# Optimization experiments

Hardware: AMD Instinct MI355X
Metric: run time of the kernel (lower is better)

Reference implementation:

```python
import jax, jax.numpy as jnp
import numpy as np

N = 10000    # nodes
D = 128      # d_model
K = 16       # d_state
S = 5        # seq_len (tokens per node)
E = 320000   # edges
R = 200      # num relation types
P = E // (S - 1)  # edges sampled per tokenizer step
EPS = 1e-5


def setup_inputs() -> dict:
    key = jax.random.key(0)
    ks = jax.random.split(key, 16)
    sc = 1.0 / np.sqrt(D)
    return {
        "x": jax.random.normal(ks[0], (N, D), jnp.float32),
        "edge_index": jax.random.randint(ks[1], (2, E), 0, N),
        "edge_type": jax.random.randint(ks[2], (E,), 0, R),
        "perms": jax.random.randint(ks[3], (S - 1, P), 0, E),
        "rel_table": jax.random.normal(ks[4], (R, D), jnp.float32) * 0.1,
        "log_A": jax.random.normal(ks[5], (D, K), jnp.float32) * 0.1,
        "W_B": jax.random.normal(ks[6], (D, K), jnp.float32) * sc,
        "W_C": jax.random.normal(ks[7], (D, K), jnp.float32) * sc,
        "W_delta": jax.random.normal(ks[8], (D, D), jnp.float32) * sc,
        "b_delta": jnp.zeros((D,), jnp.float32),
        "W_g": jax.random.normal(ks[9], (D, D), jnp.float32) * sc,
        "b_g": jnp.zeros((D,), jnp.float32),
        "W_out": jax.random.normal(ks[10], (D, D), jnp.float32) * sc,
        "b_out": jnp.zeros((D,), jnp.float32),
        "ln_g": jnp.ones((D,), jnp.float32),
        "ln_b": jnp.zeros((D,), jnp.float32),
    }


def _tokenize(x, edge_index, edge_type, perms, rel_table):
    # x: [N,D]; perms: [S-1,P] -> tokens [N,S,D]
    src, dst = edge_index[0], edge_index[1]
    step_src = src[perms]                    # [S-1,P]
    step_dst = dst[perms]                    # [S-1,P]
    msg = x[step_src] + rel_table[edge_type[perms]]  # [S-1,P,D]
    seg = jax.vmap(lambda i, m: jax.ops.segment_sum(m, i, num_segments=N))(step_dst, msg)  # [S-1,N,D]
    deg = jax.vmap(lambda i: jax.ops.segment_sum(jnp.ones((P,), x.dtype), i, num_segments=N))(step_dst)  # [S-1,N]
    neigh = seg / jnp.clip(deg, 1.0)[..., None]
    return jnp.concatenate([x[:, None, :], jnp.moveaxis(neigh, 0, 1)], axis=1)  # [N,S,D]


def _selective_scan(tokens, log_A, W_B, W_C, W_delta, b_delta):
    # tokens: [N,S,D] -> [N,S,D]
    deltas = jax.nn.softplus(tokens @ W_delta + b_delta)  # [N,S,D]
    Bs = tokens @ W_B                                     # [N,S,K]
    Cs = tokens @ W_C                                     # [N,S,K]
    A_cont = -jnp.exp(log_A)                              # [D,K]
    A_disc = jnp.exp(deltas[..., None] * A_cont)          # [N,S,D,K]
    Bx = deltas[..., None] * Bs[:, :, None, :] * tokens[..., None]  # [N,S,D,K] = B_disc * x_k

    def step(state, xs):
        a, bx, c = xs                          # [N,D,K],[N,D,K],[N,K]
        state = a * state + bx
        y = jnp.einsum('ndk,nk->nd', state, c)
        return state, y

    init = jnp.zeros((tokens.shape[0], D, K), tokens.dtype)
    _, ys = jax.lax.scan(step, init, (jnp.moveaxis(A_disc, 1, 0),
                                      jnp.moveaxis(Bx, 1, 0),
                                      jnp.moveaxis(Cs, 1, 0)))
    return jnp.moveaxis(ys, 0, 1)  # [N,S,D]


def reference(x, edge_index, edge_type, perms, rel_table, log_A, W_B, W_C,
              W_delta, b_delta, W_g, b_g, W_out, b_out, ln_g, ln_b):
    tokens = _tokenize(x, edge_index, edge_type, perms, rel_table)
    out_f = _selective_scan(tokens, log_A, W_B, W_C, W_delta, b_delta)
    out_b = _selective_scan(tokens[:, ::-1, :], log_A, W_B, W_C, W_delta, b_delta)
    scan_out = (out_f + out_b[:, ::-1, :]).mean(axis=1)  # [N,D]
    gate = jax.nn.silu(x @ W_g + b_g)
    res = x + gate * (scan_out @ W_out + b_out)
    mu = res.mean(axis=-1, keepdims=True)
    var = res.var(axis=-1, keepdims=True)
    return (res - mu) / jnp.sqrt(var + EPS) * ln_g + ln_b
```

## Files before the change

kernel.cpp:

```cpp
#include <hip/hip_runtime.h>
#include <hip/hip_bf16.h>
#include <math.h>

#define N_NODES 10000
#define D_MODEL 128
#define E_EDGES 320000
#define P_EDGES 80000
#define R_REL 200
#define LN_EPS 1e-5f
#define NBUCK 40960
#define CAP 32
#define M_ROWS 50000
#define M_PAD  50048
#define NPAD   320

typedef __attribute__((ext_vector_type(8))) short bf16x8;
typedef __attribute__((ext_vector_type(4))) float f32x4;

__device__ __forceinline__ unsigned short f2bf(float f) {
    __hip_bfloat16 h = __float2bfloat16(f);
    return *reinterpret_cast<unsigned short*>(&h);
}
__device__ __forceinline__ float bf2f(unsigned int u) {
    return __uint_as_float(u << 16);
}

__global__ __launch_bounds__(256) void prep_all(
    const float* __restrict__ Wd, const float* __restrict__ Wb,
    const float* __restrict__ Wc, const float* __restrict__ Wg,
    const float* __restrict__ W_out,
    const float* __restrict__ x, const float* __restrict__ rel,
    unsigned short* __restrict__ Bp, unsigned short* __restrict__ Wop,
    unsigned short* __restrict__ x_bf, unsigned short* __restrict__ rel_bf,
    int* __restrict__ cnt)
{
    int gid = blockIdx.x * 256 + threadIdx.x;
    if (gid < 40960) {
        int k = gid / NPAD, n = gid - (gid / NPAD) * NPAD;
        float v = 0.f;
        if (n < 128)      v = Wd[k * 128 + n];
        else if (n < 144) v = Wb[k * 16 + (n - 128)];
        else if (n < 160) v = Wc[k * 16 + (n - 144)];
        else if (n < 288) v = Wg[k * 128 + (n - 160)];
        Bp[((size_t)(k >> 3) * NPAD + n) * 8 + (k & 7)] = f2bf(v);
    } else if (gid < 57344) {
        int i = gid - 40960;
        int k = i >> 7, n = i & 127;
        Wop[((size_t)(k >> 3) * 128 + n) * 8 + (k & 7)] = f2bf(W_out[k * 128 + n]);
    } else if (gid < 98304) {
        cnt[gid - 57344] = 0;
    } else if (gid < 123904) {
        int i = gid - 98304;
        rel_bf[i] = f2bf(rel[i]);
    } else if (gid < 123904 + N_NODES * D_MODEL) {
        int i = gid - 123904;
        x_bf[i] = f2bf(x[i]);
    }
}

__global__ __launch_bounds__(256) void csr_build(
    const int* __restrict__ edge_index, const int* __restrict__ edge_type,
    const int* __restrict__ perms,
    int* __restrict__ cnt, int2* __restrict__ slots)
{
    int gid = blockIdx.x * blockDim.x + threadIdx.x;
    if (gid >= 4 * P_EDGES) return;
    int s = gid / P_EDGES;
    int e = perms[gid];
    int src = edge_index[e];
    int dst = edge_index[E_EDGES + e];
    int et  = edge_type[e];
    int b = dst * 4 + s;
    int pos = atomicAdd(&cnt[b], 1);
    if (pos < CAP) slots[(size_t)b * CAP + pos] = make_int2(src, et);
}

__global__ __launch_bounds__(256) void gather_tokens(
    const unsigned short* __restrict__ x_bf,
    const int* __restrict__ cnt, const int2* __restrict__ slots,
    const unsigned short* __restrict__ rel_bf,
    unsigned short* __restrict__ tokens)
{
    int n = blockIdx.x;
    int w = threadIdx.x >> 6, lane = threadIdx.x & 63;
    int b = n * 4 + w;
    int c = cnt[b];
    int cc = c < CAP ? c : CAP;
    const int2* sl = slots + (size_t)b * CAP;
    const unsigned int* xu = (const unsigned int*)x_bf;
    const unsigned int* ru = (const unsigned int*)rel_bf;
    float ax = 0.f, ay = 0.f;
    int j = 0;
    for (; j + 2 <= cc; j += 2) {
        int4 two = *(const int4*)(sl + j);
        unsigned int xa = xu[(size_t)two.x * 64 + lane];
        unsigned int ra = ru[(size_t)two.y * 64 + lane];
        unsigned int xb = xu[(size_t)two.z * 64 + lane];
        unsigned int rb = ru[(size_t)two.w * 64 + lane];
        ax += bf2f(xa & 0xffffu) + bf2f(ra & 0xffffu)
            + bf2f(xb & 0xffffu) + bf2f(rb & 0xffffu);
        ay += bf2f(xa >> 16) + bf2f(ra >> 16)
            + bf2f(xb >> 16) + bf2f(rb >> 16);
    }
    if (j < cc) {
        int2 se = sl[j];
        unsigned int xa = xu[(size_t)se.x * 64 + lane];
        unsigned int ra = ru[(size_t)se.y * 64 + lane];
        ax += bf2f(xa & 0xffffu) + bf2f(ra & 0xffffu);
        ay += bf2f(xa >> 16) + bf2f(ra >> 16);
    }
    float inv = 1.f / fmaxf((float)c, 1.f);
    unsigned int pack = (unsigned int)f2bf(ax * inv)
                      | ((unsigned int)f2bf(ay * inv) << 16);
    ((unsigned int*)tokens)[((size_t)n * 5 + w + 1) * 64 + lane] = pack;
    if (w == 0)
        ((unsigned int*)tokens)[((size_t)n * 5) * 64 + lane] = xu[(size_t)n * 64 + lane];
}

__global__ __launch_bounds__(256) void mfma_gemm(
    const unsigned short* __restrict__ tokens,
    const unsigned short* __restrict__ Bp,
    const float* __restrict__ b_delta, const float* __restrict__ b_g,
    unsigned short* __restrict__ delta,
    unsigned short* __restrict__ bc,
    unsigned short* __restrict__ g)
{
    int m0 = blockIdx.x * 64, n0 = blockIdx.y * 64;
    int wv = threadIdx.x >> 6, lane = threadIdx.x & 63;
    int quad = lane >> 4, l16 = lane & 15;

    f32x4 acc[4] = {{0,0,0,0},{0,0,0,0},{0,0,0,0},{0,0,0,0}};
    const unsigned short* arow = tokens + (size_t)(m0 + wv * 16 + l16) * 128 + quad * 8;
    #pragma unroll
    for (int kc = 0; kc < 128; kc += 32) {
        bf16x8 a = *(const bf16x8*)(arow + kc);
        #pragma unroll
        for (int t = 0; t < 4; ++t) {
            bf16x8 b = *(const bf16x8*)(Bp + ((size_t)(kc / 8 + quad) * NPAD + n0 + 16 * t + l16) * 8);
            acc[t] = __builtin_amdgcn_mfma_f32_16x16x32_bf16(a, b, acc[t], 0, 0, 0);
        }
    }

    int rbase = m0 + wv * 16 + quad * 4;
    #pragma unroll
    for (int t = 0; t < 4; ++t) {
        int c = n0 + 16 * t + l16;
        #pragma unroll
        for (int reg = 0; reg < 4; ++reg) {
            int r = rbase + reg;
            if (r >= M_ROWS) continue;
            float v = acc[t][reg];
            if (c < 128) {
                float z = v + b_delta[c];
                float d = (z > 15.f) ? z : log1pf(__expf(z));
                delta[(size_t)r * 128 + c] = f2bf(d);
            } else if (c < 160) {
                bc[(size_t)r * 32 + (c - 128)] = f2bf(v);
            } else if (c < 288) {
                int rq = r / 5;
                if (r - rq * 5 == 0)
                    g[(size_t)rq * 128 + (c - 160)] = f2bf(v + b_g[c - 160]);
            }
        }
    }
}

__global__ __launch_bounds__(128) void scan_so(
    const unsigned short* __restrict__ tokens,
    const unsigned short* __restrict__ delta,
    const unsigned short* __restrict__ bcbuf,
    const float* __restrict__ log_A,
    unsigned short* __restrict__ so)
{
    int n = blockIdx.x, tid = threadIdx.x;
    __shared__ __align__(16) float BC[160];

    for (int idx = tid; idx < 160; idx += 128) {
        int s = idx >> 5, q = idx & 31;
        BC[idx] = bf2f(bcbuf[((size_t)n * 5 + s) * 32 + q]);
    }
    float tv[5], dl[5];
    #pragma unroll
    for (int s = 0; s < 5; ++s) {
        tv[s] = bf2f(tokens[((size_t)n * 5 + s) * 128 + tid]);
        dl[s] = bf2f(delta[((size_t)n * 5 + s) * 128 + tid]);
    }
    float Ac[16];
    {
        const float4* la = (const float4*)(log_A + tid * 16);
        #pragma unroll
        for (int q = 0; q < 4; ++q) {
            float4 lv = la[q];
            Ac[q * 4 + 0] = -__expf(lv.x);
            Ac[q * 4 + 1] = -__expf(lv.y);
            Ac[q * 4 + 2] = -__expf(lv.z);
            Ac[q * 4 + 3] = -__expf(lv.w);
        }
    }
    __syncthreads();

    float Af[5][16];
    float total = 0.f;
    {
        float st[16];
        #pragma unroll
        for (int k = 0; k < 16; ++k) st[k] = 0.f;
        #pragma unroll
        for (int s = 0; s < 5; ++s) {
            float dtv = dl[s] * tv[s];
            float y = 0.f;
            #pragma unroll
            for (int k = 0; k < 16; ++k) {
                float A = __expf(dl[s] * Ac[k]);
                Af[s][k] = A;
                st[k] = fmaf(A, st[k], dtv * BC[s * 32 + k]);
                y = fmaf(st[k], BC[s * 32 + 16 + k], y);
            }
            total += y;
        }
    }
    {
        float st[16];
        #pragma unroll
        for (int k = 0; k < 16; ++k) st[k] = 0.f;
        #pragma unroll
        for (int s = 4; s >= 0; --s) {
            float dtv = dl[s] * tv[s];
            float y = 0.f;
            #pragma unroll
            for (int k = 0; k < 16; ++k) {
                st[k] = fmaf(Af[s][k], st[k], dtv * BC[s * 32 + k]);
                y = fmaf(st[k], BC[s * 32 + 16 + k], y);
            }
            total += y;
        }
    }
    so[(size_t)n * 128 + tid] = f2bf(total * 0.2f);
}

__global__ __launch_bounds__(256) void out_gemm(
    const unsigned short* __restrict__ so,
    const unsigned short* __restrict__ Wop,
    const unsigned short* __restrict__ gbuf,
    const float* __restrict__ x,
    const float* __restrict__ b_out,
    const float* __restrict__ ln_g, const float* __restrict__ ln_b,
    float* __restrict__ out)
{
    int m0 = blockIdx.x * 16;
    int tid = threadIdx.x;
    int wv = tid >> 6, lane = tid & 63;
    int quad = lane >> 4, l16 = lane & 15;

    __shared__ float res[16 * 132];
    __shared__ float pmu[16][16];
    __shared__ float pv2[16][16];
    __shared__ float muA[16], rstdA[16];

    f32x4 acc[2] = {{0,0,0,0},{0,0,0,0}};
    const unsigned short* arow = so + (size_t)(m0 + l16) * 128 + quad * 8;
    #pragma unroll
    for (int kc = 0; kc < 128; kc += 32) {
        bf16x8 a = *(const bf16x8*)(arow + kc);
        #pragma unroll
        for (int tt = 0; tt < 2; ++tt) {
            int t = wv * 2 + tt;
            bf16x8 b = *(const bf16x8*)(Wop + ((size_t)(kc / 8 + quad) * 128 + 16 * t + l16) * 8);
            acc[tt] = __builtin_amdgcn_mfma_f32_16x16x32_bf16(a, b, acc[tt], 0, 0, 0);
        }
    }

    #pragma unroll
    for (int tt = 0; tt < 2; ++tt) {
        int c = wv * 32 + tt * 16 + l16;
        #pragma unroll
        for (int reg = 0; reg < 4; ++reg) {
            int lrow = quad * 4 + reg;
            int r = m0 + lrow;
            float o = acc[tt][reg] + b_out[c];
            float gl = bf2f(gbuf[(size_t)r * 128 + c]);
            float gate = gl / (1.f + __expf(-gl));
            res[lrow * 132 + c] = x[(size_t)r * 128 + c] + gate * o;
        }
    }
    __syncthreads();

    {
        int row = tid >> 4, q = tid & 15;
        float s = 0.f, s2 = 0.f;
        #pragma unroll
        for (int i = 0; i < 8; ++i) {
            float v = res[row * 132 + q + 16 * i];
            s += v; s2 += v * v;
        }
        pmu[row][q] = s; pv2[row][q] = s2;
    }
    __syncthreads();
    if (tid < 16) {
        float s = 0.f, s2 = 0.f;
        #pragma unroll
        for (int i = 0; i < 16; ++i) { s += pmu[tid][i]; s2 += pv2[tid][i]; }
        float mu = s * (1.f / 128.f);
        float var = s2 * (1.f / 128.f) - mu * mu;
        muA[tid] = mu;
        rstdA[tid] = rsqrtf(var + LN_EPS);
    }
    __syncthreads();
    #pragma unroll
    for (int i = 0; i < 8; ++i) {
        int idx = i * 256 + tid;
        int row = idx >> 7, c = idx & 127;
        out[(size_t)(m0 + row) * 128 + c] =
            (res[row * 132 + c] - muA[row]) * rstdA[row] * ln_g[c] + ln_b[c];
    }
}

extern "C" void kernel_launch(void* const* d_in, const int* in_sizes, int n_in,
                              void* d_out, int out_size, void* d_ws, size_t ws_size,
                              hipStream_t stream) {
    const float* x          = (const float*)d_in[0];
    const int*   edge_index = (const int*)  d_in[1];
    const int*   edge_type  = (const int*)  d_in[2];
    const int*   perms      = (const int*)  d_in[3];
    const float* rel_table  = (const float*)d_in[4];
    const float* log_A      = (const float*)d_in[5];
    const float* W_B        = (const float*)d_in[6];
    const float* W_C        = (const float*)d_in[7];
    const float* W_delta    = (const float*)d_in[8];
    const float* b_delta    = (const float*)d_in[9];
    const float* W_g        = (const float*)d_in[10];
    const float* b_g        = (const float*)d_in[11];
    const float* W_out      = (const float*)d_in[12];
    const float* b_out      = (const float*)d_in[13];
    const float* ln_g       = (const float*)d_in[14];
    const float* ln_b       = (const float*)d_in[15];

    char* ws = (char*)d_ws;
    int*            cnt    = (int*)           (ws + 0);
    unsigned short* Bp     = (unsigned short*)(ws + 163840);
    unsigned short* Wop    = (unsigned short*)(ws + 245760);
    unsigned short* x_bf   = (unsigned short*)(ws + 278528);
    unsigned short* rel_bf = (unsigned short*)(ws + 2838528);
    unsigned short* tokens = (unsigned short*)(ws + 2889728);
    unsigned short* g      = (unsigned short*)(ws + 15702016);
    unsigned short* so     = (unsigned short*)(ws + 18262016);
    unsigned short* bc     = (unsigned short*)(ws + 20822016);
    int2*           slots  = (int2*)          (ws + 24022016);
    unsigned short* delta  = (unsigned short*)(ws + 24022016);

    prep_all<<<(123904 + N_NODES * D_MODEL + 255) / 256, 256, 0, stream>>>(
        W_delta, W_B, W_C, W_g, W_out, x, rel_table,
        Bp, Wop, x_bf, rel_bf, cnt);

    csr_build<<<(4 * P_EDGES + 255) / 256, 256, 0, stream>>>(
        edge_index, edge_type, perms, cnt, slots);

    gather_tokens<<<N_NODES, 256, 0, stream>>>(
        x_bf, cnt, slots, rel_bf, tokens);

    mfma_gemm<<<dim3(M_PAD / 64, NPAD / 64), 256, 0, stream>>>(
        tokens, Bp, b_delta, b_g, delta, bc, g);

    scan_so<<<N_NODES, 128, 0, stream>>>(
        tokens, delta, bc, log_A, so);

    out_gemm<<<N_NODES / 16, 256, 0, stream>>>(
        so, Wop, g, x, b_out, ln_g, ln_b, (float*)d_out);
}
```

Measured before the change: 204.9 us.

## Fuse selective scan into output GEMM and pack edge data into int4

Merges the per-node scan kernel into the output GEMM + layernorm kernel. Each 256-thread block now scans 16 nodes and keeps the scan output in shared memory, which removes a launch and the round trip of the scan output through global memory. It also packs src, dst and type per edge into an int4 during prep, so the CSR build does one gather instead of three. The gather loop is unrolled to four edges for more memory parallelism. In exchange, the fused kernel runs only 625 blocks doing serial per-node scan work, which may lower occupancy, and prep gains extra edge-packing traffic.

```diff
diff --git a/kernel.cpp b/kernel.cpp
--- a/kernel.cpp
+++ b/kernel.cpp
@@ -6,7 +6,6 @@
 #define D_MODEL 128
 #define E_EDGES 320000
 #define P_EDGES 80000
-#define R_REL 200
 #define LN_EPS 1e-5f
 #define NBUCK 40960
 #define CAP 32
@@ -30,9 +29,10 @@
     const float* __restrict__ Wc, const float* __restrict__ Wg,
     const float* __restrict__ W_out,
     const float* __restrict__ x, const float* __restrict__ rel,
+    const int* __restrict__ edge_index, const int* __restrict__ edge_type,
     unsigned short* __restrict__ Bp, unsigned short* __restrict__ Wop,
     unsigned short* __restrict__ x_bf, unsigned short* __restrict__ rel_bf,
-    int* __restrict__ cnt)
+    int* __restrict__ cnt, int4* __restrict__ ed4)
 {
     int gid = blockIdx.x * 256 + threadIdx.x;
     if (gid < 40960) {
@@ -52,27 +52,27 @@
     } else if (gid < 123904) {
         int i = gid - 98304;
         rel_bf[i] = f2bf(rel[i]);
-    } else if (gid < 123904 + N_NODES * D_MODEL) {
+    } else if (gid < 1403904) {
         int i = gid - 123904;
         x_bf[i] = f2bf(x[i]);
+    } else if (gid < 1723904) {
+        int e = gid - 1403904;
+        ed4[e] = make_int4(edge_index[e], edge_index[E_EDGES + e], edge_type[e], 0);
     }
 }
 
 __global__ __launch_bounds__(256) void csr_build(
-    const int* __restrict__ edge_index, const int* __restrict__ edge_type,
-    const int* __restrict__ perms,
+    const int4* __restrict__ ed4, const int* __restrict__ perms,
     int* __restrict__ cnt, int2* __restrict__ slots)
 {
     int gid = blockIdx.x * blockDim.x + threadIdx.x;
     if (gid >= 4 * P_EDGES) return;
     int s = gid / P_EDGES;
     int e = perms[gid];
-    int src = edge_index[e];
-    int dst = edge_index[E_EDGES + e];
-    int et  = edge_type[e];
-    int b = dst * 4 + s;
+    int4 ed = ed4[e];
+    int b = ed.y * 4 + s;
     int pos = atomicAdd(&cnt[b], 1);
-    if (pos < CAP) slots[(size_t)b * CAP + pos] = make_int2(src, et);
+    if (pos < CAP) slots[(size_t)b * CAP + pos] = make_int2(ed.x, ed.z);
 }
 
 __global__ __launch_bounds__(256) void gather_tokens(
@@ -91,16 +91,37 @@
     const unsigned int* ru = (const unsigned int*)rel_bf;
     float ax = 0.f, ay = 0.f;
     int j = 0;
-    for (; j + 2 <= cc; j += 2) {
-        int4 two = *(const int4*)(sl + j);
-        unsigned int xa = xu[(size_t)two.x * 64 + lane];
-        unsigned int ra = ru[(size_t)two.y * 64 + lane];
-        unsigned int xb = xu[(size_t)two.z * 64 + lane];
-        unsigned int rb = ru[(size_t)two.w * 64 + lane];
-        ax += bf2f(xa & 0xffffu) + bf2f(ra & 0xffffu)
-            + bf2f(xb & 0xffffu) + bf2f(rb & 0xffffu);
-        ay += bf2f(xa >> 16) + bf2f(ra >> 16)
-            + bf2f(xb >> 16) + bf2f(rb >> 16);
+    for (; j + 4 <= cc; j += 4) {
+        int4 e01 = *(const int4*)(sl + j);
+        int4 e23 = *(const int4*)(sl + j + 2);
+        unsigned int x0 = xu[(size_t)e01.x * 64 + lane];
+        unsigned int r0 = ru[(size_t)e01.y * 64 + lane];
+        unsigned int x1 = xu[(size_t)e01.z * 64 + lane];
+        unsigned int r1 = ru[(size_t)e01.w * 64 + lane];
+        unsigned int x2 = xu[(size_t)e23.x * 64 + lane];
+        unsigned int r2 = ru[(size_t)e23.y * 64 + lane];
+        unsigned int x3 = xu[(size_t)e23.z * 64 + lane];
+        unsigned int r3 = ru[(size_t)e23.w * 64 + lane];
+        ax += (bf2f(x0 & 0xffffu) + bf2f(r0 & 0xffffu))
+            + (bf2f(x1 & 0xffffu) + bf2f(r1 & 0xffffu))
+            + (bf2f(x2 & 0xffffu) + bf2f(r2 & 0xffffu))
+            + (bf2f(x3 & 0xffffu) + bf2f(r3 & 0xffffu));
+        ay += (bf2f(x0 >> 16) + bf2f(r0 >> 16))
+            + (bf2f(x1 >> 16) + bf2f(r1 >> 16))
+            + (bf2f(x2 >> 16) + bf2f(r2 >> 16))
+            + (bf2f(x3 >> 16) + bf2f(r3 >> 16));
+    }
+    if (j + 2 <= cc) {
+        int4 e01 = *(const int4*)(sl + j);
+        unsigned int x0 = xu[(size_t)e01.x * 64 + lane];
+        unsigned int r0 = ru[(size_t)e01.y * 64 + lane];
+        unsigned int x1 = xu[(size_t)e01.z * 64 + lane];
+        unsigned int r1 = ru[(size_t)e01.w * 64 + lane];
+        ax += (bf2f(x0 & 0xffffu) + bf2f(r0 & 0xffffu))
+            + (bf2f(x1 & 0xffffu) + bf2f(r1 & 0xffffu));
+        ay += (bf2f(x0 >> 16) + bf2f(r0 >> 16))
+            + (bf2f(x1 >> 16) + bf2f(r1 >> 16));
+        j += 2;
     }
     if (j < cc) {
         int2 se = sl[j];
@@ -165,29 +186,38 @@
     }
 }
 
-__global__ __launch_bounds__(128) void scan_so(
+__global__ __launch_bounds__(256) void scan_out(
     const unsigned short* __restrict__ tokens,
     const unsigned short* __restrict__ delta,
     const unsigned short* __restrict__ bcbuf,
     const float* __restrict__ log_A,
-    unsigned short* __restrict__ so)
-{
-    int n = blockIdx.x, tid = threadIdx.x;
-    __shared__ __align__(16) float BC[160];
-
-    for (int idx = tid; idx < 160; idx += 128) {
-        int s = idx >> 5, q = idx & 31;
-        BC[idx] = bf2f(bcbuf[((size_t)n * 5 + s) * 32 + q]);
-    }
-    float tv[5], dl[5];
-    #pragma unroll
-    for (int s = 0; s < 5; ++s) {
-        tv[s] = bf2f(tokens[((size_t)n * 5 + s) * 128 + tid]);
-        dl[s] = bf2f(delta[((size_t)n * 5 + s) * 128 + tid]);
-    }
+    const unsigned short* __restrict__ Wop,
+    const unsigned short* __restrict__ gbuf,
+    const float* __restrict__ x,
+    const float* __restrict__ b_out,
+    const float* __restrict__ ln_g, const float* __restrict__ ln_b,
+    float* __restrict__ out)
+{
+    int m0 = blockIdx.x * 16;
+    int t = threadIdx.x;
+
+    __shared__ float BCs[16][160];
+    __shared__ unsigned short soL[16][128];
+    __shared__ float res[16 * 132];
+    __shared__ float pmu[16][16];
+    __shared__ float pv2[16][16];
+    __shared__ float muA[16], rstdA[16];
+
+    for (int idx = t; idx < 2560; idx += 256) {
+        int n = idx / 160, rem = idx - n * 160;
+        int s = rem >> 5, q = rem & 31;
+        BCs[n][rem] = bf2f(bcbuf[((size_t)(m0 + n) * 5 + s) * 32 + q]);
+    }
+
+    const int d = t & 127;
     float Ac[16];
     {
-        const float4* la = (const float4*)(log_A + tid * 16);
+        const float4* la = (const float4*)(log_A + d * 16);
         #pragma unroll
         for (int q = 0; q < 4; ++q) {
             float4 lv = la[q];
@@ -199,73 +229,69 @@
     }
     __syncthreads();
 
-    float Af[5][16];
-    float total = 0.f;
-    {
-        float st[16];
-        #pragma unroll
-        for (int k = 0; k < 16; ++k) st[k] = 0.f;
+    #pragma unroll 1
+    for (int i = 0; i < 8; ++i) {
+        int n = 2 * i + (t >> 7);
+        const unsigned short* tb = tokens + ((size_t)(m0 + n) * 5) * 128 + d;
+        const unsigned short* db = delta  + ((size_t)(m0 + n) * 5) * 128 + d;
+        float tv[5], dl[5];
         #pragma unroll
         for (int s = 0; s < 5; ++s) {
-            float dtv = dl[s] * tv[s];
-            float y = 0.f;
+            tv[s] = bf2f(tb[s * 128]);
+            dl[s] = bf2f(db[s * 128]);
+        }
+        const float* BCn = BCs[n];
+
+        float Af[5][16];
+        float total = 0.f;
+        {
+            float st[16];
             #pragma unroll
-            for (int k = 0; k < 16; ++k) {
-                float A = __expf(dl[s] * Ac[k]);
-                Af[s][k] = A;
-                st[k] = fmaf(A, st[k], dtv * BC[s * 32 + k]);
-                y = fmaf(st[k], BC[s * 32 + 16 + k], y);
+            for (int k = 0; k < 16; ++k) st[k] = 0.f;
+            #pragma unroll
+            for (int s = 0; s < 5; ++s) {
+                float dtv = dl[s] * tv[s];
+                float y = 0.f;
+                #pragma unroll
+                for (int k = 0; k < 16; ++k) {
+                    float A = __expf(dl[s] * Ac[k]);
+                    Af[s][k] = A;
+                    st[k] = fmaf(A, st[k], dtv * BCn[s * 32 + k]);
+                    y = fmaf(st[k], BCn[s * 32 + 16 + k], y);
+                }
+                total += y;
             }
-            total += y;
-        }
-    }
-    {
-        float st[16];
-        #pragma unroll
-        for (int k = 0; k < 16; ++k) st[k] = 0.f;
-        #pragma unroll
-        for (int s = 4; s >= 0; --s) {
-            float dtv = dl[s] * tv[s];
-            float y = 0.f;
+        }
+        {
+            float st[16];
             #pragma unroll
-            for (int k = 0; k < 16; ++k) {
-                st[k] = fmaf(Af[s][k], st[k], dtv * BC[s * 32 + k]);
-                y = fmaf(st[k], BC[s * 32 + 16 + k], y);
+            for (int k = 0; k < 16; ++k) st[k] = 0.f;
+            #pragma unroll
+            for (int s = 4; s >= 0; --s) {
+                float dtv = dl[s] * tv[s];
+                float y = 0.f;
+                #pragma unroll
+                for (int k = 0; k < 16; ++k) {
+                    st[k] = fmaf(Af[s][k], st[k], dtv * BCn[s * 32 + k]);
+                    y = fmaf(st[k], BCn[s * 32 + 16 + k], y);
+                }
+                total += y;
             }
-            total += y;
-        }
-    }
-    so[(size_t)n * 128 + tid] = f2bf(total * 0.2f);
-}
-
-__global__ __launch_bounds__(256) void out_gemm(
-    const unsigned short* __restrict__ so,
-    const unsigned short* __restrict__ Wop,
-    const unsigned short* __restrict__ gbuf,
-    const float* __restrict__ x,
-    const float* __restrict__ b_out,
-    const float* __restrict__ ln_g, const float* __restrict__ ln_b,
-    float* __restrict__ out)
-{
-    int m0 = blockIdx.x * 16;
-    int tid = threadIdx.x;
-    int wv = tid >> 6, lane = tid & 63;
+        }
+        soL[n][d] = f2bf(total * 0.2f);
+    }
+    __syncthreads();
+
+    int wv = t >> 6, lane = t & 63;
     int quad = lane >> 4, l16 = lane & 15;
-
-    __shared__ float res[16 * 132];
-    __shared__ float pmu[16][16];
-    __shared__ float pv2[16][16];
-    __shared__ float muA[16], rstdA[16];
-
     f32x4 acc[2] = {{0,0,0,0},{0,0,0,0}};
-    const unsigned short* arow = so + (size_t)(m0 + l16) * 128 + quad * 8;
     #pragma unroll
     for (int kc = 0; kc < 128; kc += 32) {
-        bf16x8 a = *(const bf16x8*)(arow + kc);
+        bf16x8 a = *(const bf16x8*)&soL[l16][kc + quad * 8];
         #pragma unroll
         for (int tt = 0; tt < 2; ++tt) {
-            int t = wv * 2 + tt;
-            bf16x8 b = *(const bf16x8*)(Wop + ((size_t)(kc / 8 + quad) * 128 + 16 * t + l16) * 8);
+            int tc = wv * 2 + tt;
+            bf16x8 b = *(const bf16x8*)(Wop + ((size_t)(kc / 8 + quad) * 128 + 16 * tc + l16) * 8);
             acc[tt] = __builtin_amdgcn_mfma_f32_16x16x32_bf16(a, b, acc[tt], 0, 0, 0);
         }
     }
@@ -286,7 +312,7 @@
     __syncthreads();
 
     {
-        int row = tid >> 4, q = tid & 15;
+        int row = t >> 4, q = t & 15;
         float s = 0.f, s2 = 0.f;
         #pragma unroll
         for (int i = 0; i < 8; ++i) {
@@ -296,19 +322,19 @@
         pmu[row][q] = s; pv2[row][q] = s2;
     }
     __syncthreads();
-    if (tid < 16) {
+    if (t < 16) {
         float s = 0.f, s2 = 0.f;
         #pragma unroll
-        for (int i = 0; i < 16; ++i) { s += pmu[tid][i]; s2 += pv2[tid][i]; }
+        for (int i = 0; i < 16; ++i) { s += pmu[t][i]; s2 += pv2[t][i]; }
         float mu = s * (1.f / 128.f);
         float var = s2 * (1.f / 128.f) - mu * mu;
-        muA[tid] = mu;
-        rstdA[tid] = rsqrtf(var + LN_EPS);
+        muA[t] = mu;
+        rstdA[t] = rsqrtf(var + LN_EPS);
     }
     __syncthreads();
     #pragma unroll
     for (int i = 0; i < 8; ++i) {
-        int idx = i * 256 + tid;
+        int idx = i * 256 + t;
         int row = idx >> 7, c = idx & 127;
         out[(size_t)(m0 + row) * 128 + c] =
             (res[row * 132 + c] - muA[row]) * rstdA[row] * ln_g[c] + ln_b[c];
@@ -341,19 +367,19 @@
     unsigned short* Wop    = (unsigned short*)(ws + 245760);
     unsigned short* x_bf   = (unsigned short*)(ws + 278528);
     unsigned short* rel_bf = (unsigned short*)(ws + 2838528);
-    unsigned short* tokens = (unsigned short*)(ws + 2889728);
-    unsigned short* g      = (unsigned short*)(ws + 15702016);
-    unsigned short* so     = (unsigned short*)(ws + 18262016);
-    unsigned short* bc     = (unsigned short*)(ws + 20822016);
-    int2*           slots  = (int2*)          (ws + 24022016);
-    unsigned short* delta  = (unsigned short*)(ws + 24022016);
-
-    prep_all<<<(123904 + N_NODES * D_MODEL + 255) / 256, 256, 0, stream>>>(
-        W_delta, W_B, W_C, W_g, W_out, x, rel_table,
-        Bp, Wop, x_bf, rel_bf, cnt);
+    int4*           ed4    = (int4*)          (ws + 2889728);
+    unsigned short* tokens = (unsigned short*)(ws + 8009728);
+    unsigned short* g      = (unsigned short*)(ws + 20822016);
+    unsigned short* bc     = (unsigned short*)(ws + 23382016);
+    int2*           slots  = (int2*)          (ws + 26582016);
+    unsigned short* delta  = (unsigned short*)(ws + 26582016);
+
+    prep_all<<<(1723904 + 255) / 256, 256, 0, stream>>>(
+        W_delta, W_B, W_C, W_g, W_out, x, rel_table, edge_index, edge_type,
+        Bp, Wop, x_bf, rel_bf, cnt, ed4);
 
     csr_build<<<(4 * P_EDGES + 255) / 256, 256, 0, stream>>>(
-        edge_index, edge_type, perms, cnt, slots);
+        ed4, perms, cnt, slots);
 
     gather_tokens<<<N_NODES, 256, 0, stream>>>(
         x_bf, cnt, slots, rel_bf, tokens);
@@ -361,9 +387,6 @@
     mfma_gemm<<<dim3(M_PAD / 64, NPAD / 64), 256, 0, stream>>>(
         tokens, Bp, b_delta, b_g, delta, bc, g);
 
-    scan_so<<<N_NODES, 128, 0, stream>>>(
-        tokens, delta, bc, log_A, so);
-
-    out_gemm<<<N_NODES / 16, 256, 0, stream>>>(
-        so, Wop, g, x, b_out, ln_g, ln_b, (float*)d_out);
-}
+    scan_out<<<N_NODES / 16, 256, 0, stream>>>(
+        tokens, delta, bc, log_A, Wop, g, x, b_out, ln_g, ln_b, (float*)d_out);
+}
```

Result: no change. 202.4 us (-1.2%).
